# Kernel tuning notes

Measured on AMD Instinct MI355X. Metric: run time of the kernel, lower is better.

Reference implementation:

```python
import jax, jax.numpy as jnp
import numpy as np

B, S, L = 8, 512, 1536          # batch, new tokens, cached tokens
H, HQ, HKV, D = 4096, 32, 8, 128
THETA = 500000.0


def _rope(x, pos):
    # x: [b, s, h, d]; pos: [s] absolute positions. Llama half-split RoPE.
    half = D // 2
    inv_freq = 1.0 / (THETA ** (jnp.arange(half, dtype=jnp.float32) / half))
    ang = pos.astype(jnp.float32)[:, None] * inv_freq[None, :]      # [s, half]
    cos = jnp.cos(ang)[None, :, None, :]
    sin = jnp.sin(ang)[None, :, None, :]
    x1, x2 = x[..., :half], x[..., half:]
    return jnp.concatenate([x1 * cos - x2 * sin, x2 * cos + x1 * sin], axis=-1)


def setup_inputs() -> dict:
    key = jax.random.key(0)
    ks = jax.random.split(key, 7)
    return {
        "hidden_states": jax.random.normal(ks[0], (B, S, H), jnp.float32),
        "k_cache": jax.random.normal(ks[1], (B, L, HKV, D), jnp.float32),
        "v_cache": jax.random.normal(ks[2], (B, L, HKV, D), jnp.float32),
        "wq": jax.random.normal(ks[3], (H, HQ * D), jnp.float32) * (H ** -0.5),
        "wk": jax.random.normal(ks[4], (H, HKV * D), jnp.float32) * (H ** -0.5),
        "wv": jax.random.normal(ks[5], (H, HKV * D), jnp.float32) * (H ** -0.5),
        "wo": jax.random.normal(ks[6], (HQ * D, H), jnp.float32) * ((HQ * D) ** -0.5),
    }


def reference(hidden_states, k_cache, v_cache, wq, wk, wv, wo):
    b, s, _ = hidden_states.shape
    # fused QKV projections (bias=False)
    q = (hidden_states @ wq).reshape(b, s, HQ, D)
    k = (hidden_states @ wk).reshape(b, s, HKV, D)
    v = (hidden_states @ wv).reshape(b, s, HKV, D)

    pos = L + jnp.arange(s)                     # absolute positions of new tokens
    q = _rope(q, pos)
    k = _rope(k, pos)

    # append new tokens to the (already-rotated) KV cache
    K = jnp.concatenate([k_cache, k], axis=1)   # [b, T, hkv, d]
    V = jnp.concatenate([v_cache, v], axis=1)
    T = K.shape[1]

    g = HQ // HKV                               # GQA group size
    qg = q.reshape(b, s, HKV, g, D)
    scores = jnp.einsum("bskgd,btkd->bskgt", qg, K) * (D ** -0.5)

    # causal mask: query at global position L+i attends to kv position t <= L+i
    allowed = jnp.arange(T)[None, :] <= (L + jnp.arange(s))[:, None]   # [s, T]
    scores = jnp.where(allowed[None, :, None, None, :], scores, jnp.finfo(scores.dtype).min)

    attn = jax.nn.softmax(scores, axis=-1)
    out = jnp.einsum("bskgt,btkd->bskgd", attn, V).reshape(b, s, HQ * D)
    return out @ wo
```

## Files before the change

### kernel.cpp

```cpp
#include <hip/hip_runtime.h>
#include <cstdint>
#include <cstddef>

#define B_   8
#define S_   512
#define L_   1536
#define T_   2048
#define H_   4096
#define HQ_  32
#define HKV_ 8
#define D_   128

typedef __bf16 bf16;
typedef __bf16 bf16x8 __attribute__((ext_vector_type(8)));
typedef float  f32x4  __attribute__((ext_vector_type(4)));

#define LOG2_THETA 18.931568569324174f
#define SCL (0.08838834764831845f * 1.4426950408889634f)

__device__ __forceinline__ void gld_lds16(const void* g, void* l) {
    __builtin_amdgcn_global_load_lds(
        (const __attribute__((address_space(1))) void*)g,
        (__attribute__((address_space(3))) void*)l, 16, 0, 0);
}

#define BAR()                                   \
    do {                                        \
        asm volatile("" ::: "memory");          \
        __builtin_amdgcn_s_barrier();           \
        asm volatile("" ::: "memory");          \
    } while (0)

__global__ void pack_bf16(const float* __restrict__ src, bf16* __restrict__ dst, int n4) {
    int i = blockIdx.x * 256 + threadIdx.x;
    if (i >= n4) return;
    float4 v = ((const float4*)src)[i];
    bf16 h[4] = {(bf16)v.x, (bf16)v.y, (bf16)v.z, (bf16)v.w};
    *(uint2*)(dst + 4 * (size_t)i) = *(const uint2*)h;
}

__global__ void transpose_pack(const float* __restrict__ src, bf16* __restrict__ dst,
                               int N, int rowOff) {
    __shared__ float t[32][33];
    int n0 = blockIdx.x * 32, k0 = blockIdx.y * 32;
    int c = threadIdx.x & 31, r = threadIdx.x >> 5;
    for (int i = 0; i < 4; i++)
        t[r + 8 * i][c] = src[(size_t)(k0 + r + 8 * i) * N + n0 + c];
    __syncthreads();
    for (int i = 0; i < 4; i++)
        dst[(size_t)(rowOff + n0 + r + 8 * i) * 4096 + k0 + c] = (bf16)t[c][r + 8 * i];
}

template <bool OUT_BF16>
__global__ __launch_bounds__(512, 2) void gemm256(const bf16* __restrict__ A,
                                                  const bf16* __restrict__ Bt,
                                                  void* __restrict__ Cv,
                                                  int M, int N, int K) {
    __shared__ alignas(16) bf16 As[2][256 * 64];
    __shared__ alignas(16) bf16 Bs[2][256 * 64];

    const int tid = threadIdx.x, lane = tid & 63;
    const int wid = tid >> 6, wm = wid >> 2, wn = wid & 3;
    const int l15 = lane & 15, q4 = lane >> 4;

    const int m0 = blockIdx.y * 256, n0 = blockIdx.x * 256;
    const int nkt = K >> 6;
    const int NITER = K >> 7;

    const int scs = (((tid & 7) ^ ((tid >> 3) & 7)) * 8);
    const size_t offg0 = (size_t)(tid >> 3) * K + scs;
    const size_t offg1 = offg0 + (size_t)64 * K;
    const int lds0 = (tid & ~63) * 8;
    const int lds1 = lds0 + 4096;

    const bf16* Ag = A + (size_t)m0 * K;
    const bf16* Bg = Bt + (size_t)n0 * K;

    const int swz = l15 & 7;
    const int cc0 = ((0 + q4) ^ swz) * 8;
    const int cc1 = ((4 + q4) ^ swz) * 8;

#define ST(G, ARR, BUF, H, KT)                                                \
    if ((KT) < nkt) {                                                         \
        gld_lds16(G + (size_t)(H) * 128 * K + (size_t)(KT) * 64 + offg0,      \
                  &ARR[BUF][(H) * 8192 + lds0]);                              \
        gld_lds16(G + (size_t)(H) * 128 * K + (size_t)(KT) * 64 + offg1,      \
                  &ARR[BUF][(H) * 8192 + lds1]);                              \
    }

#define RDA(BUF, MH)                                                           \
    _Pragma("unroll") for (int mi = 0; mi < 4; ++mi) {                         \
        const bf16* p = &As[BUF][(wm * 128 + (MH) * 64 + mi * 16 + l15) * 64]; \
        afr[mi][0] = *(const bf16x8*)(p + cc0);                                \
        afr[mi][1] = *(const bf16x8*)(p + cc1);                                \
    }

#define RDB(BUF, NH)                                                           \
    _Pragma("unroll") for (int ni = 0; ni < 2; ++ni) {                         \
        const bf16* p = &Bs[BUF][(wn * 64 + (NH) * 32 + ni * 16 + l15) * 64];  \
        bfr[NH][ni][0] = *(const bf16x8*)(p + cc0);                            \
        bfr[NH][ni][1] = *(const bf16x8*)(p + cc1);                            \
    }

#define MM(MH, NH)                                                             \
    __builtin_amdgcn_s_setprio(1);                                             \
    _Pragma("unroll") for (int mi = 0; mi < 4; ++mi)                           \
    _Pragma("unroll") for (int ni = 0; ni < 2; ++ni) {                         \
        acc[(MH)*4 + mi][(NH)*2 + ni] = __builtin_amdgcn_mfma_f32_16x16x32_bf16( \
            afr[mi][0], bfr[NH][ni][0], acc[(MH)*4 + mi][(NH)*2 + ni], 0, 0, 0); \
        acc[(MH)*4 + mi][(NH)*2 + ni] = __builtin_amdgcn_mfma_f32_16x16x32_bf16( \
            afr[mi][1], bfr[NH][ni][1], acc[(MH)*4 + mi][(NH)*2 + ni], 0, 0, 0); \
    }                                                                          \
    __builtin_amdgcn_s_setprio(0);

    f32x4 acc[8][4];
#pragma unroll
    for (int i = 0; i < 8; ++i)
#pragma unroll
        for (int j = 0; j < 4; ++j) acc[i][j] = (f32x4){0.f, 0.f, 0.f, 0.f};

    bf16x8 afr[4][2];
    bf16x8 bfr[2][2][2];

    ST(Bg, Bs, 0, 0, 0); ST(Bg, Bs, 0, 1, 0);
    ST(Ag, As, 0, 0, 0); ST(Ag, As, 0, 1, 0);
    ST(Bg, Bs, 1, 0, 1); ST(Bg, Bs, 1, 1, 1);
    asm volatile("s_waitcnt vmcnt(4)" ::: "memory");
    BAR();

    for (int it = 0; it < NITER; ++it) {
        const int t1 = 2 * it + 1, t2 = 2 * it + 2, t3 = 2 * it + 3;
        RDA(0, 0); RDB(0, 0); ST(Ag, As, 1, 0, t1); BAR(); MM(0, 0); BAR();
        RDB(0, 1);            ST(Ag, As, 1, 1, t1); BAR(); MM(0, 1); BAR();
        RDA(0, 1);            ST(Bg, Bs, 0, 0, t2); BAR(); MM(1, 0); BAR();
                              ST(Bg, Bs, 0, 1, t2); BAR(); MM(1, 1);
        if (it == NITER - 1) {
            asm volatile("s_waitcnt vmcnt(0)" ::: "memory");
        } else {
            asm volatile("s_waitcnt vmcnt(4)" ::: "memory");
        }
        BAR();
        RDA(1, 0); RDB(1, 0); ST(Ag, As, 0, 0, t2); BAR(); MM(0, 0); BAR();
        RDB(1, 1);            ST(Ag, As, 0, 1, t2); BAR(); MM(0, 1); BAR();
        RDA(1, 1);            ST(Bg, Bs, 1, 0, t3); BAR(); MM(1, 0); BAR();
                              ST(Bg, Bs, 1, 1, t3); BAR(); MM(1, 1);
        asm volatile("s_waitcnt vmcnt(4)" ::: "memory");
        BAR();
    }

    const int colb = n0 + wn * 64 + l15;
    const int rowb = m0 + wm * 128 + q4 * 4;
#pragma unroll
    for (int mi = 0; mi < 8; ++mi)
#pragma unroll
        for (int ni = 0; ni < 4; ++ni)
#pragma unroll
            for (int r = 0; r < 4; ++r) {
                size_t row = (size_t)(rowb + mi * 16 + r);
                size_t col = (size_t)(colb + ni * 16);
                if (OUT_BF16)
                    ((bf16*)Cv)[row * N + col] = (bf16)acc[mi][ni][r];
                else
                    ((float*)Cv)[row * N + col] = acc[mi][ni][r];
            }
#undef ST
#undef RDA
#undef RDB
#undef MM
}

__device__ __forceinline__ float rope_val(const bf16* row, int d, int pos) {
    int i = d & 63;
    float inv = exp2f(-(float)i * (LOG2_THETA / 64.0f));
    float ang = (float)pos * inv;
    float sn, cs;
    sincosf(ang, &sn, &cs);
    float x = (float)row[d];
    float xo = (float)row[(d < 64) ? d + 64 : d - 64];
    return (d < 64) ? x * cs - xo * sn : x * cs + xo * sn;
}

__global__ void rope_q(const bf16* __restrict__ qkv, bf16* __restrict__ Qb) {
    size_t idx = (size_t)blockIdx.x * 256 + threadIdx.x;
    int d = idx & 127;
    int h = (idx >> 7) & 31;
    int m = idx >> 12;
    int s = m & 511;
    const bf16* row = qkv + (size_t)m * 6144 + h * 128;
    Qb[idx] = (bf16)(rope_val(row, d, L_ + s) * SCL);
}

__global__ void build_k(const bf16* __restrict__ qkv, const float* __restrict__ kcache,
                        bf16* __restrict__ Kf) {
    size_t idx = (size_t)blockIdx.x * 256 + threadIdx.x;
    int d = idx & 127;
    int hk = (idx >> 7) & 7;
    int t = (idx >> 10) & 2047;
    int b = idx >> 21;
    if (t < L_) {
        Kf[idx] = (bf16)kcache[(((size_t)b * L_ + t) * HKV_ + hk) * D_ + d];
    } else {
        int s = t - L_;
        const bf16* row = qkv + (size_t)(b * S_ + s) * 6144 + 4096 + hk * 128;
        Kf[idx] = (bf16)rope_val(row, d, t);
    }
}

__global__ void build_vT(const bf16* __restrict__ qkv, const float* __restrict__ vcache,
                         bf16* __restrict__ VtG) {
    __shared__ float tile[32][33];
    int t0 = blockIdx.x * 32, d0 = blockIdx.y * 32, z = blockIdx.z;
    int b = z >> 3, hk = z & 7;
    int c = threadIdx.x & 31, r = threadIdx.x >> 5;
    if (t0 < L_) {
        for (int i = 0; i < 4; i++)
            tile[r + 8 * i][c] =
                vcache[(((size_t)b * L_ + t0 + r + 8 * i) * HKV_ + hk) * D_ + d0 + c];
    } else {
        for (int i = 0; i < 4; i++)
            tile[r + 8 * i][c] =
                (float)qkv[(size_t)(b * S_ + t0 - L_ + r + 8 * i) * 6144 + 5120 + hk * 128 + d0 + c];
    }
    __syncthreads();
    for (int i = 0; i < 4; i++)
        VtG[((size_t)(b * 8 + hk) * 128 + d0 + r + 8 * i) * T_ + t0 + c] = (bf16)tile[c][r + 8 * i];
}

__global__ __launch_bounds__(256) void attn(const bf16* __restrict__ Q,
                                            const bf16* __restrict__ Kf,
                                            const bf16* __restrict__ VtG,
                                            bf16* __restrict__ Ao) {
    __shared__ alignas(16) bf16 Kl[64 * 128];
    __shared__ alignas(16) bf16 Vl[128 * 64];
    __shared__ alignas(16) bf16 Pl[4 * 32 * 64];

    int tid = threadIdx.x, lane = tid & 63, w = tid >> 6;
    int l15 = lane & 15, q4 = lane >> 4;
    int bid = blockIdx.x;
    int b = bid & 7, hk = (bid >> 3) & 7, scb = bid >> 6;
    int s0 = scb * 32;
    int sbw = s0 + w * 8;
    int swz = l15 & 7;

    bf16x8 qf[2][4];
    for (int mt = 0; mt < 2; mt++) {
        int s_q = sbw + mt * 4 + (l15 >> 2);
        int h = hk * 4 + (l15 & 3);
        const bf16* qp = Q + (((size_t)(b * S_ + s_q) * HQ_ + h) << 7);
        for (int kc = 0; kc < 4; kc++) qf[mt][kc] = *(const bf16x8*)(qp + kc * 32 + q4 * 8);
    }

    f32x4 O[2][8];
    float lsum[2][4];
    for (int mt = 0; mt < 2; mt++) {
        for (int dt = 0; dt < 8; dt++) O[mt][dt] = (f32x4){0.f, 0.f, 0.f, 0.f};
        for (int r = 0; r < 4; r++) lsum[mt][r] = 0.f;
    }

    int ntiles = (L_ + s0 + 32 + 63) >> 6;
    const bf16* Kbase = Kf + ((size_t)b * T_ * HKV_ + hk) * D_;
    const bf16* Vbase = VtG + (size_t)(b * 8 + hk) * 128 * T_;

    for (int tile = 0; tile < ntiles; ++tile) {
        int t0 = tile << 6;
        for (int it = 0; it < 4; it++) {
            int ci = it * 256 + tid;
            int key = ci >> 4, c = ci & 15, sc = c ^ (key & 7);
            gld_lds16(Kbase + (size_t)(t0 + key) * (HKV_ * D_) + sc * 8, &Kl[(ci & ~63) * 8]);
        }
        for (int it = 0; it < 4; it++) {
            int ci = it * 256 + tid;
            int row = ci >> 3, c = ci & 7, sc = c ^ (row & 7);
            gld_lds16(Vbase + (size_t)row * T_ + t0 + sc * 8, &Vl[(ci & ~63) * 8]);
        }
        __syncthreads();

        if (t0 <= L_ + sbw + 7) {
            f32x4 sv[2][4];
            for (int mt = 0; mt < 2; mt++)
                for (int kg = 0; kg < 4; kg++) sv[mt][kg] = (f32x4){0.f, 0.f, 0.f, 0.f};
            for (int kg = 0; kg < 4; kg++) {
                bf16x8 kfr[4];
                int krow = kg * 16 + l15;
                for (int kc = 0; kc < 4; kc++)
                    kfr[kc] = *(const bf16x8*)&Kl[krow * 128 + (((kc * 4 + q4) ^ swz) * 8)];
                for (int mt = 0; mt < 2; mt++)
                    for (int kc = 0; kc < 4; kc++)
                        sv[mt][kg] = __builtin_amdgcn_mfma_f32_16x16x32_bf16(
                            qf[mt][kc], kfr[kc], sv[mt][kg], 0, 0, 0);
            }
            bool need_mask = (t0 + 63 > L_ + sbw);
            for (int mt = 0; mt < 2; mt++) {
                int lim = L_ + sbw + mt * 4 + q4;
                for (int kg = 0; kg < 4; kg++) {
                    int tK = t0 + kg * 16 + l15;
                    for (int r = 0; r < 4; r++) {
                        float z = sv[mt][kg][r];
                        if (need_mask && tK > lim) z = -3.0e38f;
                        z = __builtin_amdgcn_exp2f(z);
                        lsum[mt][r] += z;
                        int rr = mt * 16 + q4 * 4 + r;
                        int cpos = (kg * 2 + (l15 >> 3)) ^ (rr & 7);
                        Pl[w * 2048 + rr * 64 + cpos * 8 + (l15 & 7)] = (bf16)z;
                    }
                }
            }
            for (int kcv = 0; kcv < 2; kcv++) {
                bf16x8 pf[2];
                for (int mt = 0; mt < 2; mt++)
                    pf[mt] = *(const bf16x8*)&Pl[w * 2048 + (mt * 16 + l15) * 64 +
                                                 (((kcv * 4 + q4) ^ swz) * 8)];
                for (int dt = 0; dt < 8; dt++) {
                    bf16x8 vfr = *(const bf16x8*)&Vl[(dt * 16 + l15) * 64 +
                                                     (((kcv * 4 + q4) ^ swz) * 8)];
                    for (int mt = 0; mt < 2; mt++)
                        O[mt][dt] = __builtin_amdgcn_mfma_f32_16x16x32_bf16(
                            pf[mt], vfr, O[mt][dt], 0, 0, 0);
                }
            }
        }
        __syncthreads();
    }

    for (int mt = 0; mt < 2; mt++)
        for (int r = 0; r < 4; r++) {
            float v = lsum[mt][r];
            for (int off = 1; off < 16; off <<= 1) v += __shfl_xor(v, off, 16);
            lsum[mt][r] = 1.f / v;
        }
    for (int mt = 0; mt < 2; mt++) {
        int s = sbw + mt * 4 + q4;
        for (int r = 0; r < 4; r++) {
            size_t base = (((size_t)(b * S_ + s) * HQ_ + hk * 4 + r) << 7);
            for (int dt = 0; dt < 8; dt++)
                Ao[base + dt * 16 + l15] = (bf16)(O[mt][dt][r] * lsum[mt][r]);
        }
    }
}

extern "C" void kernel_launch(void* const* d_in, const int* in_sizes, int n_in,
                              void* d_out, int out_size, void* d_ws, size_t ws_size,
                              hipStream_t stream) {
    const float* hs = (const float*)d_in[0];
    const float* kc = (const float*)d_in[1];
    const float* vc = (const float*)d_in[2];
    const float* wq = (const float*)d_in[3];
    const float* wk = (const float*)d_in[4];
    const float* wv = (const float*)d_in[5];
    const float* wo = (const float*)d_in[6];
    float* out = (float*)d_out;
    char* ws = (char*)d_ws;

    const size_t SZ_HB   = (size_t)4096 * 4096 * 2;
    const size_t SZ_WQKV = (size_t)6144 * 4096 * 2;
    const size_t SZ_WO   = (size_t)4096 * 4096 * 2;
    const size_t SZ_QKV  = (size_t)4096 * 6144 * 2;
    const size_t SZ_Q    = (size_t)4096 * 4096 * 2;
    const size_t SZ_KV   = (size_t)B_ * T_ * HKV_ * D_ * 2;

    bf16* hb    = (bf16*)(ws);
    bf16* wqkvt = (bf16*)(ws + SZ_HB);
    bf16* wot   = (bf16*)(ws + SZ_HB + SZ_WQKV);
    bf16* qkv   = (bf16*)(ws + SZ_HB + SZ_WQKV + SZ_WO);
    bf16* qb    = (bf16*)(ws + SZ_HB + SZ_WQKV + SZ_WO + SZ_QKV);
    bf16* kf    = (bf16*)(ws + SZ_HB + SZ_WQKV + SZ_WO + SZ_QKV + SZ_Q);
    bf16* vtg   = (bf16*)(ws + SZ_HB + SZ_WQKV + SZ_WO + SZ_QKV + SZ_Q + SZ_KV);
    bf16* ao    = hb;

    pack_bf16<<<16384, 256, 0, stream>>>(hs, hb, 4096 * 4096 / 4);
    transpose_pack<<<dim3(128, 128), 256, 0, stream>>>(wq, wqkvt, 4096, 0);
    transpose_pack<<<dim3(32, 128), 256, 0, stream>>>(wk, wqkvt, 1024, 4096);
    transpose_pack<<<dim3(32, 128), 256, 0, stream>>>(wv, wqkvt, 1024, 5120);
    transpose_pack<<<dim3(128, 128), 256, 0, stream>>>(wo, wot, 4096, 0);
    gemm256<true><<<dim3(24, 16), 512, 0, stream>>>(hb, wqkvt, qkv, 4096, 6144, 4096);
    rope_q<<<65536, 256, 0, stream>>>(qkv, qb);
    build_k<<<65536, 256, 0, stream>>>(qkv, kc, kf);
    build_vT<<<dim3(64, 4, 64), 256, 0, stream>>>(qkv, vc, vtg);
    attn<<<1024, 256, 0, stream>>>(qb, kf, vtg, ao);
    gemm256<false><<<dim3(16, 16), 512, 0, stream>>>(ao, wot, out, 4096, 4096, 4096);
}
```

Before: 987.3 us.

## Deepen GEMM prefetch so both A and B tiles load a full stage ahead

```diff
diff --git a/kernel.cpp b/kernel.cpp
--- a/kernel.cpp
+++ b/kernel.cpp
@@ -29,6 +29,12 @@
         asm volatile("" ::: "memory");          \
         __builtin_amdgcn_s_barrier();           \
         asm volatile("" ::: "memory");          \
+    } while (0)
+
+#define WAIT_LGKM()                                          \
+    do {                                                     \
+        asm volatile("s_waitcnt lgkmcnt(0)" ::: "memory");   \
+        __builtin_amdgcn_sched_barrier(0);                   \
     } while (0)
 
 __global__ void pack_bf16(const float* __restrict__ src, bf16* __restrict__ dst, int n4) {
@@ -125,26 +131,35 @@
     ST(Bg, Bs, 0, 0, 0); ST(Bg, Bs, 0, 1, 0);
     ST(Ag, As, 0, 0, 0); ST(Ag, As, 0, 1, 0);
     ST(Bg, Bs, 1, 0, 1); ST(Bg, Bs, 1, 1, 1);
-    asm volatile("s_waitcnt vmcnt(4)" ::: "memory");
+    ST(Ag, As, 1, 0, 1); ST(Ag, As, 1, 1, 1);
+    asm volatile("s_waitcnt vmcnt(8)" ::: "memory");
     BAR();
 
     for (int it = 0; it < NITER; ++it) {
-        const int t1 = 2 * it + 1, t2 = 2 * it + 2, t3 = 2 * it + 3;
-        RDA(0, 0); RDB(0, 0); ST(Ag, As, 1, 0, t1); BAR(); MM(0, 0); BAR();
-        RDB(0, 1);            ST(Ag, As, 1, 1, t1); BAR(); MM(0, 1); BAR();
-        RDA(0, 1);            ST(Bg, Bs, 0, 0, t2); BAR(); MM(1, 0); BAR();
-                              ST(Bg, Bs, 0, 1, t2); BAR(); MM(1, 1);
+        const int t2 = 2 * it + 2, t3 = 2 * it + 3;
+        RDA(0, 0); RDB(0, 0);
+        BAR(); WAIT_LGKM(); MM(0, 0); BAR();
+        RDB(0, 1);
+        BAR(); WAIT_LGKM(); MM(0, 1); BAR();
+        RDA(0, 1); ST(Bg, Bs, 0, 0, t2); ST(Bg, Bs, 0, 1, t2);
+        BAR(); WAIT_LGKM(); MM(1, 0); BAR();
+        ST(Ag, As, 0, 0, t2); ST(Ag, As, 0, 1, t2);
+        BAR(); MM(1, 1);
         if (it == NITER - 1) {
             asm volatile("s_waitcnt vmcnt(0)" ::: "memory");
         } else {
-            asm volatile("s_waitcnt vmcnt(4)" ::: "memory");
+            asm volatile("s_waitcnt vmcnt(8)" ::: "memory");
         }
         BAR();
-        RDA(1, 0); RDB(1, 0); ST(Ag, As, 0, 0, t2); BAR(); MM(0, 0); BAR();
-        RDB(1, 1);            ST(Ag, As, 0, 1, t2); BAR(); MM(0, 1); BAR();
-        RDA(1, 1);            ST(Bg, Bs, 1, 0, t3); BAR(); MM(1, 0); BAR();
-                              ST(Bg, Bs, 1, 1, t3); BAR(); MM(1, 1);
-        asm volatile("s_waitcnt vmcnt(4)" ::: "memory");
+        RDA(1, 0); RDB(1, 0);
+        BAR(); WAIT_LGKM(); MM(0, 0); BAR();
+        RDB(1, 1);
+        BAR(); WAIT_LGKM(); MM(0, 1); BAR();
+        RDA(1, 1); ST(Bg, Bs, 1, 0, t3); ST(Bg, Bs, 1, 1, t3);
+        BAR(); WAIT_LGKM(); MM(1, 0); BAR();
+        ST(Ag, As, 1, 0, t3); ST(Ag, As, 1, 1, t3);
+        BAR(); MM(1, 1);
+        asm volatile("s_waitcnt vmcnt(8)" ::: "memory");
         BAR();
     }
 
```

Result: no change. 989.8 us (+0.3%).
